# Optimization experiments

Hardware: AMD Instinct MI355X
Metric: run time of the kernel (lower is better)

## Reference

```python
import jax, jax.numpy as jnp
import numpy as np

N_NODES = 100000
N_EDGES = 3200000
D_IN = 128
D_OUT = 128


def setup_inputs() -> dict:
    key = jax.random.key(0)
    k1, k2, k3, k4, k5, k6 = jax.random.split(key, 6)
    x = jax.random.normal(k1, (N_NODES, D_IN), dtype=jnp.float32)
    weight = jax.random.normal(k2, (D_OUT, D_IN), dtype=jnp.float32)
    bias = jax.random.normal(k3, (D_OUT,), dtype=jnp.float32)
    edge_vals = jax.random.uniform(k4, (N_EDGES,), dtype=jnp.float32)
    edge_rows = jax.random.randint(k5, (N_EDGES,), 0, N_NODES, dtype=jnp.int32)
    edge_cols = jax.random.randint(k6, (N_EDGES,), 0, N_NODES, dtype=jnp.int32)
    return {"x": x, "weight": weight, "bias": bias,
            "edge_vals": edge_vals, "edge_rows": edge_rows, "edge_cols": edge_cols}


def reference(x, weight, bias, edge_vals, edge_rows, edge_cols):
    # h = Linear(x): [N, D_OUT]
    h = jnp.einsum('ni,oi->no', x, weight) + bias
    # out = A @ h with A in COO form: out[r] += v * h[c]
    msgs = edge_vals[:, None] * h[edge_cols]  # [E, D_OUT]
    out = jax.ops.segment_sum(msgs, edge_rows, num_segments=N_NODES)
    return out
```

## Files before the change

### kernel.cpp

```cpp
#include <hip/hip_runtime.h>
#include <hip/hip_bf16.h>

#define D 128
#define RPB 256
#define RPB_SHIFT 8
#define NBMAX 512
#define P1CHUNK 8192
#define CAP 9216
#define OVFCAP 4096

using bf16x8 = __attribute__((ext_vector_type(8))) short;
using f32x4  = __attribute__((ext_vector_type(4))) float;
using f32x2  = __attribute__((ext_vector_type(2))) float;

static __device__ inline unsigned short f2bf(float f) {
    __hip_bfloat16 b = __float2bfloat16(f);
    return reinterpret_cast<unsigned short&>(b);
}

__global__ __launch_bounds__(256) void gemm_pass1_kernel(
    const float* __restrict__ x, const float* __restrict__ W,
    const float* __restrict__ bias, __hip_bfloat16* __restrict__ h, int N,
    const int* __restrict__ rows, const int* __restrict__ cols,
    const float* __restrict__ vals,
    int* __restrict__ bcount,
    uint2* __restrict__ pairs,
    uint4* __restrict__ ovf,
    int NB, int E, int GB, int HB)
{
    __shared__ __align__(16) char smem[48 * 1024];
    const int tid = threadIdx.x;

    const int T   = GB + HB;
    const int bid = blockIdx.x;
    const int p_before = (int)(((long long)bid * HB) / T);
    const int p_after  = (int)(((long long)(bid + 1) * HB) / T);

    if (p_after > p_before) {
        int* srows = reinterpret_cast<int*>(smem);
        int* lh    = reinterpret_cast<int*>(smem + 32 * 1024);
        int* lbase = reinterpret_cast<int*>(smem + 34 * 1024);

        const int base = p_before * P1CHUNK;

        for (int i = tid; i < NBMAX; i += 256) lh[i] = 0;
        __syncthreads();

#pragma unroll 4
        for (int it = 0; it < P1CHUNK / 256; ++it) {
            int e = base + it * 256 + tid;
            int r = (e < E) ? rows[e] : -1;
            srows[it * 256 + tid] = r;
            if (r >= 0) atomicAdd(&lh[r >> RPB_SHIFT], 1);
        }
        __syncthreads();

        for (int i = tid; i < NBMAX; i += 256) {
            int c = lh[i];
            lbase[i] = c ? (i * CAP + atomicAdd(&bcount[i], c)) : 0;
            lh[i] = 0;
        }
        __syncthreads();

#pragma unroll 4
        for (int it = 0; it < P1CHUNK / 256; ++it) {
            int e = base + it * 256 + tid;
            int r = srows[it * 256 + tid];
            if (r < 0) continue;
            int b = r >> RPB_SHIFT;
            int lofs = atomicAdd(&lh[b], 1);
            int pos = lbase[b] + lofs;
            if (pos < (b + 1) * CAP) {
                unsigned packed = ((unsigned)(r & (RPB - 1)) << 17) | (unsigned)cols[e];
                pairs[pos] = make_uint2(packed, __float_as_uint(vals[e]));
            } else {
                int oi = atomicAdd(&bcount[NB], 1);
                if (oi < OVFCAP)
                    ovf[oi] = make_uint4((unsigned)r, (unsigned)cols[e],
                                         __float_as_uint(vals[e]), 0u);
            }
        }
        return;
    }

    const int gb = bid - p_before;
    char* sA = smem;
    char* sB = smem + 16 * 1024;
    const int nbase = gb * 64;

#pragma unroll
    for (int it = 0; it < 16; ++it) {
        const int r = it * 8 + (tid >> 5);
        const int c = (tid & 31) * 4;
        const unsigned addr = (unsigned)((r * 256 + c * 2) ^ ((r & 7) << 4));

        float4 wv = *reinterpret_cast<const float4*>(W + (size_t)r * D + c);
        ushort4 wb = make_ushort4(f2bf(wv.x), f2bf(wv.y), f2bf(wv.z), f2bf(wv.w));
        *reinterpret_cast<ushort4*>(sB + addr) = wb;

        if (it < 8) {
            const int gr = nbase + r;
            float4 xv = make_float4(0.f, 0.f, 0.f, 0.f);
            if (gr < N) xv = *reinterpret_cast<const float4*>(x + (size_t)gr * D + c);
            ushort4 xb = make_ushort4(f2bf(xv.x), f2bf(xv.y), f2bf(xv.z), f2bf(xv.w));
            *reinterpret_cast<ushort4*>(sA + addr) = xb;
        }
    }
    __syncthreads();

    const int wid  = tid >> 6;
    const int lane = tid & 63;
    const int wr   = (wid >> 1) * 32;
    const int wc   = (wid & 1) * 64;
    const int lrow = lane & 15;
    const int lkb  = (lane >> 4) * 16;

    f32x4 acc[2][4] = {};

#pragma unroll
    for (int kk = 0; kk < 4; ++kk) {
        const int kbyte = kk * 64 + lkb;
        bf16x8 a[2], b[4];
#pragma unroll
        for (int m = 0; m < 2; ++m) {
            const int row = wr + m * 16 + lrow;
            const unsigned addr = (unsigned)((row * 256 + kbyte) ^ ((row & 7) << 4));
            a[m] = *reinterpret_cast<const bf16x8*>(sA + addr);
        }
#pragma unroll
        for (int n = 0; n < 4; ++n) {
            const int row = wc + n * 16 + lrow;
            const unsigned addr = (unsigned)((row * 256 + kbyte) ^ ((row & 7) << 4));
            b[n] = *reinterpret_cast<const bf16x8*>(sB + addr);
        }
#pragma unroll
        for (int m = 0; m < 2; ++m)
#pragma unroll
            for (int n = 0; n < 4; ++n)
                acc[m][n] = __builtin_amdgcn_mfma_f32_16x16x32_bf16(a[m], b[n], acc[m][n], 0, 0, 0);
    }

    float bv[4];
#pragma unroll
    for (int n = 0; n < 4; ++n) bv[n] = bias[wc + n * 16 + lrow];

#pragma unroll
    for (int m = 0; m < 2; ++m) {
        const int row0 = nbase + wr + m * 16 + (lane >> 4) * 4;
#pragma unroll
        for (int n = 0; n < 4; ++n) {
            const int col = wc + n * 16 + lrow;
#pragma unroll
            for (int r = 0; r < 4; ++r) {
                const int grow = row0 + r;
                if (grow < N)
                    h[(size_t)grow * D + col] = __float2bfloat16(acc[m][n][r] + bv[n]);
            }
        }
    }
}

__global__ __launch_bounds__(256) void pass2_fixed_kernel(
    uint2* __restrict__ pairs, const int* __restrict__ bcount,
    int* __restrict__ rowstart, int* __restrict__ rowend, int N)
{
    __shared__ uint2 st[CAP];
    __shared__ int rh[RPB];
    __shared__ int sc[RPB];
    __shared__ int cur[RPB];

    const int b   = blockIdx.x;
    const int tid = threadIdx.x;
    const int start = b * CAP;
    int cnt = bcount[b];
    if (cnt > CAP) cnt = CAP;

    rh[tid] = 0;
    __syncthreads();

    for (int i = tid; i < cnt; i += 256) {
        uint2 p = pairs[start + i];
        st[i] = p;
        atomicAdd(&rh[p.x >> 17], 1);
    }
    __syncthreads();

    int myc = rh[tid];
    sc[tid] = myc;
    __syncthreads();
    for (int off = 1; off < 256; off <<= 1) {
        int t = (tid >= off) ? sc[tid - off] : 0;
        __syncthreads();
        sc[tid] += t;
        __syncthreads();
    }
    int excl = sc[tid] - myc;
    cur[tid] = start + excl;
    int grow = b * RPB + tid;
    if (grow < N) {
        rowstart[grow] = start + excl;
        rowend[grow]   = start + excl + myc;
    }
    __syncthreads();

    for (int i = tid; i < cnt; i += 256) {
        uint2 p = st[i];
        int r = (int)(p.x >> 17);
        int pos = atomicAdd(&cur[r], 1);
        pairs[pos] = make_uint2(p.x & 0x1FFFFu, p.y);
    }
}

__global__ __launch_bounds__(256) void row_gather2_kernel(
    const __hip_bfloat16* __restrict__ hbf, const uint2* __restrict__ pairs,
    const int* __restrict__ rowstart, const int* __restrict__ rowend,
    float* __restrict__ out, int N)
{
    int row  = (int)((blockIdx.x * (size_t)blockDim.x + threadIdx.x) >> 6);
    int lane = threadIdx.x & 63;
    if (row >= N) return;

    int start = rowstart[row];
    int end   = rowend[row];

    const char* hb = reinterpret_cast<const char*>(hbf);
    const unsigned lbyte = (unsigned)lane << 2;
    float ax = 0.f, ay = 0.f;

    for (int e0 = start; e0 < end; e0 += 64) {
        int pl = e0 + lane;
        if (pl >= end) pl = end - 1;
        uint2 p = pairs[pl];
        int pc = (int)p.x, pv = (int)p.y;
        int m = end - e0; if (m > 64) m = 64;

        int idx = 0;
        const int m16 = m & ~15;
        for (; idx < m16; idx += 16) {
            unsigned c[16], vb[16], hv[16];
#pragma unroll
            for (int u = 0; u < 16; ++u) {
                c[u]  = (unsigned)__builtin_amdgcn_readlane(pc, idx + u);
                vb[u] = (unsigned)__builtin_amdgcn_readlane(pv, idx + u);
            }
#pragma unroll
            for (int u = 0; u < 16; ++u)
                hv[u] = *reinterpret_cast<const unsigned*>(hb + (((size_t)c[u]) << 8) + lbyte);
#pragma unroll
            for (int u = 0; u < 16; ++u) {
                float v = __uint_as_float(vb[u]);
                ax += v * __uint_as_float(hv[u] << 16);
                ay += v * __uint_as_float(hv[u] & 0xffff0000u);
            }
        }
        const int m8 = m & ~7;
        for (; idx < m8; idx += 8) {
            unsigned c[8], vb[8], hv[8];
#pragma unroll
            for (int u = 0; u < 8; ++u) {
                c[u]  = (unsigned)__builtin_amdgcn_readlane(pc, idx + u);
                vb[u] = (unsigned)__builtin_amdgcn_readlane(pv, idx + u);
            }
#pragma unroll
            for (int u = 0; u < 8; ++u)
                hv[u] = *reinterpret_cast<const unsigned*>(hb + (((size_t)c[u]) << 8) + lbyte);
#pragma unroll
            for (int u = 0; u < 8; ++u) {
                float v = __uint_as_float(vb[u]);
                ax += v * __uint_as_float(hv[u] << 16);
                ay += v * __uint_as_float(hv[u] & 0xffff0000u);
            }
        }
        for (; idx < m; ++idx) {
            unsigned c  = (unsigned)__builtin_amdgcn_readlane(pc, idx);
            unsigned vb = (unsigned)__builtin_amdgcn_readlane(pv, idx);
            unsigned hv = *reinterpret_cast<const unsigned*>(hb + (((size_t)c) << 8) + lbyte);
            float v = __uint_as_float(vb);
            ax += v * __uint_as_float(hv << 16);
            ay += v * __uint_as_float(hv & 0xffff0000u);
        }
    }

    f32x2 r2 = { ax, ay };
    __builtin_nontemporal_store(r2, reinterpret_cast<f32x2*>(out + (size_t)row * D) + lane);
}

__global__ __launch_bounds__(256) void fixup_kernel(
    const uint4* __restrict__ ovf, const int* __restrict__ ovfcnt,
    const __hip_bfloat16* __restrict__ hbf, float* __restrict__ out, int N)
{
    int cnt = *ovfcnt;
    if (cnt > OVFCAP) cnt = OVFCAP;
    const int wid  = threadIdx.x >> 6;
    const int lane = threadIdx.x & 63;
    const unsigned short* hb = reinterpret_cast<const unsigned short*>(hbf);
    for (int i = wid; i < cnt; i += 4) {
        uint4 e = ovf[i];
        if ((int)e.x >= N) continue;
        unsigned hv = *reinterpret_cast<const unsigned*>(hb + (size_t)e.y * D + lane * 2);
        float v = __uint_as_float(e.z);
        atomicAdd(out + (size_t)e.x * D + lane * 2,     v * __uint_as_float(hv << 16));
        atomicAdd(out + (size_t)e.x * D + lane * 2 + 1, v * __uint_as_float(hv & 0xffff0000u));
    }
}


__global__ __launch_bounds__(256) void gemm_kernel(
    const float* __restrict__ x, const float* __restrict__ W,
    const float* __restrict__ bias, float* __restrict__ h, int N)
{
    __shared__ float sWt[D][D];
    __shared__ float sx[16][D];
    const int tid = threadIdx.x;
    for (int idx = tid; idx < D * D; idx += 256) {
        int o = idx >> 7, i = idx & (D - 1);
        sWt[i][o] = W[idx];
    }
    const int nbase = blockIdx.x * 16;
    for (int idx = tid; idx < 16 * D; idx += 256) {
        int r = idx >> 7, i = idx & (D - 1);
        int n = nbase + r;
        sx[r][i] = (n < N) ? x[(size_t)n * D + i] : 0.0f;
    }
    __syncthreads();
    const int c = tid & (D - 1);
    const int rg = tid >> 7;
    float acc[8];
#pragma unroll
    for (int k = 0; k < 8; ++k) acc[k] = 0.0f;
#pragma unroll 4
    for (int i = 0; i < D; ++i) {
        float w = sWt[i][c];
#pragma unroll
        for (int k = 0; k < 8; ++k) acc[k] += sx[rg * 8 + k][i] * w;
    }
    const float b = bias[c];
#pragma unroll
    for (int k = 0; k < 8; ++k) {
        int n = nbase + rg * 8 + k;
        if (n < N) h[(size_t)n * D + c] = acc[k] + b;
    }
}

__global__ __launch_bounds__(256) void scatter_kernel(
    const float* __restrict__ h, const float* __restrict__ vals,
    const int* __restrict__ rows, const int* __restrict__ cols,
    float* __restrict__ out, int E)
{
    const int wid  = (int)((blockIdx.x * (size_t)blockDim.x + threadIdx.x) >> 6);
    const int lane = threadIdx.x & 63;
    if (wid >= E) return;
    const int   r = rows[wid];
    const int   c = cols[wid];
    const float v = vals[wid];
    float2 hv = *reinterpret_cast<const float2*>(h + (size_t)c * D + lane * 2);
    atomicAdd(out + (size_t)r * D + lane * 2,     v * hv.x);
    atomicAdd(out + (size_t)r * D + lane * 2 + 1, v * hv.y);
}

static inline size_t align16(size_t x) { return (x + 15) & ~(size_t)15; }

extern "C" void kernel_launch(void* const* d_in, const int* in_sizes, int n_in,
                              void* d_out, int out_size, void* d_ws, size_t ws_size,
                              hipStream_t stream)
{
    const float* x    = (const float*)d_in[0];
    const float* W    = (const float*)d_in[1];
    const float* bias = (const float*)d_in[2];
    const float* vals = (const float*)d_in[3];
    const int*   rows = (const int*)d_in[4];
    const int*   cols = (const int*)d_in[5];

    const int N = in_sizes[0] / D;
    const int E = in_sizes[3];
    float* out = (float*)d_out;

    const int NB = (N + RPB - 1) / RPB;
    const int GB = (N + 63) / 64;
    const int HB = (E + P1CHUNK - 1) / P1CHUNK;

    size_t f_h      = 0;
    size_t f_pairs  = f_h      + align16((size_t)N * D * 2);
    size_t f_rs     = f_pairs  + align16((size_t)NB * CAP * 8);
    size_t f_re     = f_rs     + align16((size_t)N * 4);
    size_t f_bcount = f_re     + align16((size_t)N * 4);
    size_t f_ovf    = f_bcount + align16((size_t)(NB + 1) * 4);
    size_t need_fast = f_ovf   + align16((size_t)OVFCAP * 16);

    if (ws_size >= need_fast && NB <= NBMAX && N <= (1 << 17)) {
        char* ws = (char*)d_ws;
        __hip_bfloat16* hbf = (__hip_bfloat16*)(ws + f_h);
        uint2* pairs        = (uint2*)(ws + f_pairs);
        int*   rowstart     = (int*)(ws + f_rs);
        int*   rowend       = (int*)(ws + f_re);
        int*   bcount       = (int*)(ws + f_bcount);
        uint4* ovf          = (uint4*)(ws + f_ovf);

        hipMemsetAsync(bcount, 0, (size_t)(NB + 1) * 4, stream);

        gemm_pass1_kernel<<<GB + HB, 256, 0, stream>>>(
            x, W, bias, hbf, N, rows, cols, vals, bcount, pairs, ovf, NB, E, GB, HB);

        pass2_fixed_kernel<<<NB, 256, 0, stream>>>(pairs, bcount, rowstart, rowend, N);

        int gblocks = (int)(((size_t)N * 64 + 255) / 256);
        row_gather2_kernel<<<gblocks, 256, 0, stream>>>(hbf, pairs, rowstart, rowend, out, N);

        fixup_kernel<<<1, 256, 0, stream>>>(ovf, bcount + NB, hbf, out, N);
    } else {
        float* h = (float*)d_ws;
        hipMemsetAsync(out, 0, (size_t)out_size * sizeof(float), stream);
        gemm_kernel<<<(N + 15) / 16, 256, 0, stream>>>(x, W, bias, h, N);
        scatter_kernel<<<(E + 3) / 4, 256, 0, stream>>>(h, vals, rows, cols, out, E);
    }
}
```

Before: 201.9 us.

## Pre-convert x and W to bf16 and stage GEMM tiles via global_load_lds

```diff
diff --git a/kernel.cpp b/kernel.cpp
--- a/kernel.cpp
+++ b/kernel.cpp
@@ -1,5 +1,6 @@
 #include <hip/hip_runtime.h>
 #include <hip/hip_bf16.h>
+#include <cstdint>
 
 #define D 128
 #define RPB 256
@@ -12,20 +13,54 @@
 using bf16x8 = __attribute__((ext_vector_type(8))) short;
 using f32x4  = __attribute__((ext_vector_type(4))) float;
 using f32x2  = __attribute__((ext_vector_type(2))) float;
+using s16x8  = __attribute__((ext_vector_type(8))) short;
 
 static __device__ inline unsigned short f2bf(float f) {
     __hip_bfloat16 b = __float2bfloat16(f);
     return reinterpret_cast<unsigned short&>(b);
 }
 
-__global__ __launch_bounds__(256) void gemm_pass1_kernel(
+#if defined(__has_builtin)
+#if __has_builtin(__builtin_amdgcn_global_load_lds)
+#define HAS_GLL 1
+#endif
+#endif
+
+#ifdef HAS_GLL
+static __device__ __forceinline__ void gll16(const void* g, void* l) {
+    __builtin_amdgcn_global_load_lds(
+        (const __attribute__((address_space(1))) unsigned int*)(uintptr_t)g,
+        (__attribute__((address_space(3))) unsigned int*)(uintptr_t)l,
+        16, 0, 0);
+}
+#endif
+
+__global__ __launch_bounds__(256) void precvt_kernel(
     const float* __restrict__ x, const float* __restrict__ W,
+    unsigned short* __restrict__ xbf, unsigned short* __restrict__ wbf,
+    long xc8, long wc8)
+{
+    long total = xc8 + wc8;
+    for (long i = blockIdx.x * 256L + threadIdx.x; i < total;
+         i += (long)gridDim.x * 256L) {
+        const float* src; unsigned short* dst; long j;
+        if (i < xc8) { src = x; dst = xbf; j = i; }
+        else         { src = W; dst = wbf; j = i - xc8; }
+        float4 a = *reinterpret_cast<const float4*>(src + j * 8);
+        float4 b = *reinterpret_cast<const float4*>(src + j * 8 + 4);
+        ushort4 lo = make_ushort4(f2bf(a.x), f2bf(a.y), f2bf(a.z), f2bf(a.w));
+        ushort4 hi = make_ushort4(f2bf(b.x), f2bf(b.y), f2bf(b.z), f2bf(b.w));
+        *reinterpret_cast<ushort4*>(dst + j * 8)     = lo;
+        *reinterpret_cast<ushort4*>(dst + j * 8 + 4) = hi;
+    }
+}
+
+__global__ __launch_bounds__(256) void gemm_pass1_bf_kernel(
+    const unsigned short* __restrict__ xbf, const unsigned short* __restrict__ wbf,
     const float* __restrict__ bias, __hip_bfloat16* __restrict__ h, int N,
     const int* __restrict__ rows, const int* __restrict__ cols,
     const float* __restrict__ vals,
-    int* __restrict__ bcount,
-    uint2* __restrict__ pairs,
-    uint4* __restrict__ ovf,
+    int* __restrict__ bcount, uint2* __restrict__ pairs, uint4* __restrict__ ovf,
     int NB, int E, int GB, int HB)
 {
     __shared__ __align__(16) char smem[48 * 1024];
@@ -87,6 +122,169 @@
     char* sA = smem;
     char* sB = smem + 16 * 1024;
     const int nbase = gb * 64;
+    const int wid  = tid >> 6;
+    const int lane = tid & 63;
+
+#ifdef HAS_GLL
+    if (nbase + 64 <= N) {
+        const int row_in = lane >> 4;
+        const int u      = lane & 15;
+#pragma unroll
+        for (int i = 0; i < 8; ++i) {
+            int k   = wid * 8 + i;
+            int row = k * 4 + row_in;
+            int su  = u ^ (row & 7);
+            gll16(wbf + row * D + su * 8, sB + k * 1024);
+        }
+#pragma unroll
+        for (int i = 0; i < 4; ++i) {
+            int k   = wid * 4 + i;
+            int row = k * 4 + row_in;
+            int su  = u ^ (row & 7);
+            gll16(xbf + (size_t)(nbase + row) * D + su * 8, sA + k * 1024);
+        }
+    } else
+#endif
+    {
+#pragma unroll
+        for (int i = 0; i < 8; ++i) {
+            int g = i * 256 + tid;
+            int row = g >> 4, u = g & 15;
+            unsigned addr = (unsigned)(row * 256 + ((u ^ (row & 7)) << 4));
+            *reinterpret_cast<s16x8*>(sB + addr) =
+                *reinterpret_cast<const s16x8*>(wbf + row * D + u * 8);
+        }
+#pragma unroll
+        for (int i = 0; i < 4; ++i) {
+            int g = i * 256 + tid;
+            int row = g >> 4, u = g & 15;
+            unsigned addr = (unsigned)(row * 256 + ((u ^ (row & 7)) << 4));
+            int gr = nbase + row;
+            s16x8 v = {};
+            if (gr < N)
+                v = *reinterpret_cast<const s16x8*>(xbf + (size_t)gr * D + u * 8);
+            *reinterpret_cast<s16x8*>(sA + addr) = v;
+        }
+    }
+    __syncthreads();
+
+    const int wr   = (wid >> 1) * 32;
+    const int wc   = (wid & 1) * 64;
+    const int lrow = lane & 15;
+    const int lkb  = (lane >> 4) * 16;
+
+    f32x4 acc[2][4] = {};
+
+#pragma unroll
+    for (int kk = 0; kk < 4; ++kk) {
+        const int kbyte = kk * 64 + lkb;
+        bf16x8 a[2], b[4];
+#pragma unroll
+        for (int m = 0; m < 2; ++m) {
+            const int row = wr + m * 16 + lrow;
+            const unsigned addr = (unsigned)((row * 256 + kbyte) ^ ((row & 7) << 4));
+            a[m] = *reinterpret_cast<const bf16x8*>(sA + addr);
+        }
+#pragma unroll
+        for (int n = 0; n < 4; ++n) {
+            const int row = wc + n * 16 + lrow;
+            const unsigned addr = (unsigned)((row * 256 + kbyte) ^ ((row & 7) << 4));
+            b[n] = *reinterpret_cast<const bf16x8*>(sB + addr);
+        }
+#pragma unroll
+        for (int m = 0; m < 2; ++m)
+#pragma unroll
+            for (int n = 0; n < 4; ++n)
+                acc[m][n] = __builtin_amdgcn_mfma_f32_16x16x32_bf16(a[m], b[n], acc[m][n], 0, 0, 0);
+    }
+
+    float bv[4];
+#pragma unroll
+    for (int n = 0; n < 4; ++n) bv[n] = bias[wc + n * 16 + lrow];
+
+#pragma unroll
+    for (int m = 0; m < 2; ++m) {
+        const int row0 = nbase + wr + m * 16 + (lane >> 4) * 4;
+#pragma unroll
+        for (int n = 0; n < 4; ++n) {
+            const int col = wc + n * 16 + lrow;
+#pragma unroll
+            for (int r = 0; r < 4; ++r) {
+                const int grow = row0 + r;
+                if (grow < N)
+                    h[(size_t)grow * D + col] = __float2bfloat16(acc[m][n][r] + bv[n]);
+            }
+        }
+    }
+}
+
+__global__ __launch_bounds__(256) void gemm_pass1_kernel(
+    const float* __restrict__ x, const float* __restrict__ W,
+    const float* __restrict__ bias, __hip_bfloat16* __restrict__ h, int N,
+    const int* __restrict__ rows, const int* __restrict__ cols,
+    const float* __restrict__ vals,
+    int* __restrict__ bcount, uint2* __restrict__ pairs, uint4* __restrict__ ovf,
+    int NB, int E, int GB, int HB)
+{
+    __shared__ __align__(16) char smem[48 * 1024];
+    const int tid = threadIdx.x;
+
+    const int T   = GB + HB;
+    const int bid = blockIdx.x;
+    const int p_before = (int)(((long long)bid * HB) / T);
+    const int p_after  = (int)(((long long)(bid + 1) * HB) / T);
+
+    if (p_after > p_before) {
+        int* srows = reinterpret_cast<int*>(smem);
+        int* lh    = reinterpret_cast<int*>(smem + 32 * 1024);
+        int* lbase = reinterpret_cast<int*>(smem + 34 * 1024);
+
+        const int base = p_before * P1CHUNK;
+
+        for (int i = tid; i < NBMAX; i += 256) lh[i] = 0;
+        __syncthreads();
+
+#pragma unroll 4
+        for (int it = 0; it < P1CHUNK / 256; ++it) {
+            int e = base + it * 256 + tid;
+            int r = (e < E) ? rows[e] : -1;
+            srows[it * 256 + tid] = r;
+            if (r >= 0) atomicAdd(&lh[r >> RPB_SHIFT], 1);
+        }
+        __syncthreads();
+
+        for (int i = tid; i < NBMAX; i += 256) {
+            int c = lh[i];
+            lbase[i] = c ? (i * CAP + atomicAdd(&bcount[i], c)) : 0;
+            lh[i] = 0;
+        }
+        __syncthreads();
+
+#pragma unroll 4
+        for (int it = 0; it < P1CHUNK / 256; ++it) {
+            int e = base + it * 256 + tid;
+            int r = srows[it * 256 + tid];
+            if (r < 0) continue;
+            int b = r >> RPB_SHIFT;
+            int lofs = atomicAdd(&lh[b], 1);
+            int pos = lbase[b] + lofs;
+            if (pos < (b + 1) * CAP) {
+                unsigned packed = ((unsigned)(r & (RPB - 1)) << 17) | (unsigned)cols[e];
+                pairs[pos] = make_uint2(packed, __float_as_uint(vals[e]));
+            } else {
+                int oi = atomicAdd(&bcount[NB], 1);
+                if (oi < OVFCAP)
+                    ovf[oi] = make_uint4((unsigned)r, (unsigned)cols[e],
+                                         __float_as_uint(vals[e]), 0u);
+            }
+        }
+        return;
+    }
+
+    const int gb = bid - p_before;
+    char* sA = smem;
+    char* sB = smem + 16 * 1024;
+    const int nbase = gb * 64;
 
 #pragma unroll
     for (int it = 0; it < 16; ++it) {
@@ -379,22 +577,59 @@
     const int GB = (N + 63) / 64;
     const int HB = (E + P1CHUNK - 1) / P1CHUNK;
 
-    size_t f_h      = 0;
-    size_t f_pairs  = f_h      + align16((size_t)N * D * 2);
-    size_t f_rs     = f_pairs  + align16((size_t)NB * CAP * 8);
-    size_t f_re     = f_rs     + align16((size_t)N * 4);
-    size_t f_bcount = f_re     + align16((size_t)N * 4);
-    size_t f_ovf    = f_bcount + align16((size_t)(NB + 1) * 4);
-    size_t need_fast = f_ovf   + align16((size_t)OVFCAP * 16);
-
-    if (ws_size >= need_fast && NB <= NBMAX && N <= (1 << 17)) {
+    size_t t1_xbf    = 0;
+    size_t t1_wbf    = t1_xbf    + align16((size_t)N * D * 2);
+    size_t t1_h      = t1_wbf    + align16((size_t)D * D * 2);
+    size_t t1_pairs  = t1_h      + align16((size_t)N * D * 2);
+    size_t t1_rs     = t1_pairs  + align16((size_t)NB * CAP * 8);
+    size_t t1_re     = t1_rs     + align16((size_t)N * 4);
+    size_t t1_bcount = t1_re     + align16((size_t)N * 4);
+    size_t t1_ovf    = t1_bcount + align16((size_t)(NB + 1) * 4);
+    size_t need_t1   = t1_ovf    + align16((size_t)OVFCAP * 16);
+
+    size_t t2_h      = 0;
+    size_t t2_pairs  = t2_h      + align16((size_t)N * D * 2);
+    size_t t2_rs     = t2_pairs  + align16((size_t)NB * CAP * 8);
+    size_t t2_re     = t2_rs     + align16((size_t)N * 4);
+    size_t t2_bcount = t2_re     + align16((size_t)N * 4);
+    size_t t2_ovf    = t2_bcount + align16((size_t)(NB + 1) * 4);
+    size_t need_t2   = t2_ovf    + align16((size_t)OVFCAP * 16);
+
+    if (ws_size >= need_t1 && NB <= NBMAX && N <= (1 << 17) && (N * D) % 8 == 0) {
         char* ws = (char*)d_ws;
-        __hip_bfloat16* hbf = (__hip_bfloat16*)(ws + f_h);
-        uint2* pairs        = (uint2*)(ws + f_pairs);
-        int*   rowstart     = (int*)(ws + f_rs);
-        int*   rowend       = (int*)(ws + f_re);
-        int*   bcount       = (int*)(ws + f_bcount);
-        uint4* ovf          = (uint4*)(ws + f_ovf);
+        unsigned short* xbf = (unsigned short*)(ws + t1_xbf);
+        unsigned short* wbf = (unsigned short*)(ws + t1_wbf);
+        __hip_bfloat16* hbf = (__hip_bfloat16*)(ws + t1_h);
+        uint2* pairs        = (uint2*)(ws + t1_pairs);
+        int*   rowstart     = (int*)(ws + t1_rs);
+        int*   rowend       = (int*)(ws + t1_re);
+        int*   bcount       = (int*)(ws + t1_bcount);
+        uint4* ovf          = (uint4*)(ws + t1_ovf);
+
+        hipMemsetAsync(bcount, 0, (size_t)(NB + 1) * 4, stream);
+
+        long xc8 = (long)N * D / 8;
+        long wc8 = (long)D * D / 8;
+        precvt_kernel<<<2048, 256, 0, stream>>>(x, W, xbf, wbf, xc8, wc8);
+
+        gemm_pass1_bf_kernel<<<GB + HB, 256, 0, stream>>>(
+            xbf, wbf, bias, hbf, N, rows, cols, vals,
+            bcount, pairs, ovf, NB, E, GB, HB);
+
+        pass2_fixed_kernel<<<NB, 256, 0, stream>>>(pairs, bcount, rowstart, rowend, N);
+
+        int gblocks = (int)(((size_t)N * 64 + 255) / 256);
+        row_gather2_kernel<<<gblocks, 256, 0, stream>>>(hbf, pairs, rowstart, rowend, out, N);
+
+        fixup_kernel<<<1, 256, 0, stream>>>(ovf, bcount + NB, hbf, out, N);
+    } else if (ws_size >= need_t2 && NB <= NBMAX && N <= (1 << 17)) {
+        char* ws = (char*)d_ws;
+        __hip_bfloat16* hbf = (__hip_bfloat16*)(ws + t2_h);
+        uint2* pairs        = (uint2*)(ws + t2_pairs);
+        int*   rowstart     = (int*)(ws + t2_rs);
+        int*   rowend       = (int*)(ws + t2_re);
+        int*   bcount       = (int*)(ws + t2_bcount);
+        uint4* ovf          = (uint4*)(ws + t2_ovf);
 
         hipMemsetAsync(bcount, 0, (size_t)(NB + 1) * 4, stream);
 
```

Result: no change. 205.7 us (+1.9%).
